# Optimization experiments

Measured on AMD Instinct MI355X. Metric: run time of the kernel, lower is better.

Reference implementation:

```python
import jax, jax.numpy as jnp
import numpy as np

B, L, DC, DQ, H = 32, 1024, 1024, 1024, 512
NEG_NUM = -10000.0


def setup_inputs() -> dict:
    key = jax.random.key(0)
    ks = jax.random.split(key, 7)
    s1 = 1.0 / np.sqrt(DC + DQ)
    s2 = 1.0 / np.sqrt(H)
    return {
        "ctx": jax.random.normal(ks[0], (B, L, DC), jnp.float32),
        "query": jax.random.normal(ks[1], (B, DQ), jnp.float32),
        "mask": jnp.ones((B, L), jnp.int32),
        "noise": jax.random.normal(ks[2], (B, L), jnp.float32),
        "W1": jax.random.uniform(ks[3], (DC + DQ, H), jnp.float32, -s1, s1),
        "b1": jax.random.uniform(ks[4], (H,), jnp.float32, -s1, s1),
        "w2": jax.random.uniform(ks[5], (H,), jnp.float32, -s2, s2),
        "b2": jnp.zeros((), jnp.float32),
    }


def reference(ctx, query, mask, noise, W1, b1, w2, b2):
    b, l, dc = ctx.shape
    # concat([ctx, query_expanded]) @ W1 == ctx @ W1[:DC] + query @ W1[DC:]
    hidden = jnp.tanh(
        jnp.einsum("blc,ch->blh", ctx, W1[:dc])
        + (query @ W1[dc:])[:, None, :]
        + b1
    )  # [B, L, H]
    score = hidden @ w2 + b2  # [B, L]
    score = jnp.where(mask == 0, NEG_NUM, score)
    score = score + noise  # sigmoid_noise=True -> coefficient 1
    p = jax.nn.sigmoid(score)  # p_choose_i [B, L]

    # initial prev_att: one-hot at position 0
    prev_att = jnp.zeros((b, l), score.dtype).at[:, 0].set(1.0)
    # shifted (1 - p): [1, 1-p_0, ..., 1-p_{L-2}]
    shifted = jnp.concatenate(
        [jnp.ones((b, 1), p.dtype), 1.0 - p[:, :-1]], axis=1
    )

    # linear recurrence a_t = shifted_t * a_{t-1} + prev_att_t  (a_{-1}=0)
    def step(carry, xs):
        s_t, pr_t = xs
        a = s_t * carry + pr_t
        return a, a

    _, att_t = jax.lax.scan(step, jnp.zeros((b,), p.dtype), (shifted.T, prev_att.T))
    att = att_t.T * p  # [B, L]

    expected_ctx = jnp.einsum("bl,blc->bc", att, ctx)  # bmm(p_ctx[:,None,:], ctx)
    return expected_ctx, att
```

## Files before the change

### kernel.cpp

```cpp
#include <hip/hip_runtime.h>
#include <hip/hip_bf16.h>
#include <math.h>

constexpr int Bb = 32;
constexpr int Ll = 1024;
constexpr int DC = 1024;
constexpr int DQ = 1024;
constexpr int Hh = 512;
#define NEG_NUM -10000.0f

typedef __attribute__((ext_vector_type(8))) short bf16x8;
typedef __attribute__((ext_vector_type(4))) float f32x4;

#define GLOAD_LDS16(g, l)                                                  \
    __builtin_amdgcn_global_load_lds(                                      \
        (const __attribute__((address_space(1))) void*)(g),                \
        (__attribute__((address_space(3))) void*)(l), 16, 0, 0)

__device__ inline unsigned short f2bf(float f) {
    unsigned int x = __float_as_uint(f);
    unsigned int r = (x + 0x7FFFu + ((x >> 16) & 1u)) >> 16;
    return (unsigned short)r;
}
__device__ inline float bfu(unsigned short u) {
    return __uint_as_float(((unsigned int)u) << 16);
}


__global__ __launch_bounds__(256) void prep_kernel(const float* __restrict__ W1,
                                                   const float* __restrict__ query,
                                                   const float* __restrict__ b1,
                                                   const float* __restrict__ ctx,
                                                   unsigned short* __restrict__ w1t,
                                                   float* __restrict__ qb,
                                                   float* __restrict__ score,
                                                   float* __restrict__ out_ctx,
                                                   unsigned short* __restrict__ ctxb) {
    __shared__ float red[4][64];
    const int bid = blockIdx.x;
    if (bid < 2048) {
        int idx = bid * 256 + threadIdx.x;
        int n = idx >> 10, k = idx & 1023;
        int ks = k ^ ((n & 7) << 3);
        w1t[(size_t)n * 1024 + ks] = f2bf(W1[(size_t)k * Hh + n]);
    } else if (bid < 2176) {
        int i = (bid - 2048) * 256 + threadIdx.x;
        out_ctx[i] = 0.f;
        score[i] = 0.f;
    } else if (bid < 2432) {
        const int qbid = bid - 2176;
        const int b  = qbid >> 3;
        const int hg = qbid & 7;
        const int hl = threadIdx.x & 63;
        const int j  = threadIdx.x >> 6;
        const int h  = hg * 64 + hl;
        const float* q = query + (size_t)b * DQ + j * 256;
        const float* w = W1 + (size_t)(DC + j * 256) * Hh + h;
        float a0 = 0.f, a1 = 0.f, a2 = 0.f, a3 = 0.f;
#pragma unroll 4
        for (int c = 0; c < 256; c += 4) {
            a0 += q[c + 0] * w[(size_t)(c + 0) * Hh];
            a1 += q[c + 1] * w[(size_t)(c + 1) * Hh];
            a2 += q[c + 2] * w[(size_t)(c + 2) * Hh];
            a3 += q[c + 3] * w[(size_t)(c + 3) * Hh];
        }
        red[j][hl] = (a0 + a1) + (a2 + a3);
        __syncthreads();
        if (j == 0)
            qb[(size_t)b * Hh + h] = red[0][hl] + red[1][hl] + red[2][hl] + red[3][hl] + b1[h];
    } else {
        size_t i = (size_t)((bid - 2432) * 256 + threadIdx.x) * 8;
        int row = (int)(i >> 10);
        int col = (int)(i & 1023);
        float4 v0 = *(const float4*)(ctx + i);
        float4 v1 = *(const float4*)(ctx + i + 4);
        union { unsigned short us[8]; uint4 v; } o;
        o.us[0] = f2bf(v0.x); o.us[1] = f2bf(v0.y); o.us[2] = f2bf(v0.z); o.us[3] = f2bf(v0.w);
        o.us[4] = f2bf(v1.x); o.us[5] = f2bf(v1.y); o.us[6] = f2bf(v1.z); o.us[7] = f2bf(v1.w);
        *(uint4*)(ctxb + ((size_t)row << 10) + (col ^ ((row & 7) << 3))) = o.v;
    }
}

__global__ __launch_bounds__(512, 1) void gemm_mfma(const unsigned short* __restrict__ ctxb,
                                                    const unsigned short* __restrict__ w1t,
                                                    const float* __restrict__ qb,
                                                    const float* __restrict__ w2,
                                                    float* __restrict__ score) {
    __shared__ unsigned short lds[2 * 32768];

    const int bid = blockIdx.x;
    const int n0 = ((bid >> 3) & 1) * 256;
    const int m0 = (((bid >> 4) << 3) | (bid & 7)) * 256;

    const int tid = threadIdx.x;
    const int wv = tid >> 6, lane = tid & 63;
    const int wr = wv >> 2, wc = wv & 3;
    const int lr = lane & 15, lk = lane >> 4;

    char* ldsB = (char*)lds;
    const char* ctxB = (const char*)ctxb;
    const char* w1tB = (const char*)w1t;

    const int srow = tid >> 3;
    const int scolb = (tid & 7) * 16;
    const int x = (lr & 7) << 4;

    f32x4 acc[8][4];
#pragma unroll
    for (int mf = 0; mf < 8; ++mf)
#pragma unroll
        for (int nf = 0; nf < 4; ++nf) acc[mf][nf] = (f32x4){0.f, 0.f, 0.f, 0.f};

#pragma unroll
    for (int i = 0; i < 4; ++i) {
        int row = i * 64 + srow;
        GLOAD_LDS16(ctxB + (size_t)(m0 + row) * 2048 + scolb,
                    ldsB + i * 8192 + tid * 16);
        GLOAD_LDS16(w1tB + (size_t)(n0 + row) * 2048 + scolb,
                    ldsB + 32768 + i * 8192 + tid * 16);
    }

    for (int ks = 0; ks < 16; ++ks) {
        const int cur = ks & 1;
        char* bufc = ldsB + cur * 65536;

        __builtin_amdgcn_s_barrier();
        if (ks < 15) {
            char* bufn = ldsB + (cur ^ 1) * 65536;
            const int kb = (ks + 1) * 128;
#pragma unroll
            for (int i = 0; i < 4; ++i) {
                int row = i * 64 + srow;
                GLOAD_LDS16(ctxB + (size_t)(m0 + row) * 2048 + kb + scolb,
                            bufn + i * 8192 + tid * 16);
                GLOAD_LDS16(w1tB + (size_t)(n0 + row) * 2048 + kb + scolb,
                            bufn + 32768 + i * 8192 + tid * 16);
            }
            asm volatile("s_waitcnt vmcnt(8)" ::: "memory");
        } else {
            asm volatile("s_waitcnt vmcnt(0)" ::: "memory");
        }
        __builtin_amdgcn_sched_barrier(0);
        __builtin_amdgcn_s_barrier();

#pragma unroll
        for (int kk = 0; kk < 2; ++kk) {
            const int colb = (kk * 64 + lk * 16) ^ x;
            bf16x8 a[8], bb[4];
#pragma unroll
            for (int nf = 0; nf < 4; ++nf)
                bb[nf] = *(const bf16x8*)(bufc + 32768 + (wc * 64 + nf * 16 + lr) * 128 + colb);
#pragma unroll
            for (int mf = 0; mf < 8; ++mf)
                a[mf] = *(const bf16x8*)(bufc + (wr * 128 + mf * 16 + lr) * 128 + colb);
#pragma unroll
            for (int mf = 0; mf < 8; ++mf)
#pragma unroll
                for (int nf = 0; nf < 4; ++nf)
                    acc[mf][nf] = __builtin_amdgcn_mfma_f32_16x16x32_bf16(a[mf], bb[nf], acc[mf][nf], 0, 0, 0);
        }
    }

    const int bq = m0 >> 10;
    const float* qbb = qb + (size_t)bq * Hh;
#pragma unroll
    for (int mf = 0; mf < 8; ++mf) {
        float s0 = 0.f, s1 = 0.f, s2 = 0.f, s3 = 0.f;
#pragma unroll
        for (int nf = 0; nf < 4; ++nf) {
            int col = n0 + wc * 64 + nf * 16 + lr;
            float wvw = w2[col];
            float qv = qbb[col];
            s0 += tanhf(acc[mf][nf][0] + qv) * wvw;
            s1 += tanhf(acc[mf][nf][1] + qv) * wvw;
            s2 += tanhf(acc[mf][nf][2] + qv) * wvw;
            s3 += tanhf(acc[mf][nf][3] + qv) * wvw;
        }
#pragma unroll
        for (int off = 8; off; off >>= 1) {
            s0 += __shfl_xor(s0, off, 16);
            s1 += __shfl_xor(s1, off, 16);
            s2 += __shfl_xor(s2, off, 16);
            s3 += __shfl_xor(s3, off, 16);
        }
        if (lr == 0) {
            int row = m0 + wr * 128 + mf * 16 + lk * 4;
            atomicAdd(&score[row + 0], s0);
            atomicAdd(&score[row + 1], s1);
            atomicAdd(&score[row + 2], s2);
            atomicAdd(&score[row + 3], s3);
        }
    }
}

__global__ __launch_bounds__(256) void ectx_fused(const unsigned short* __restrict__ ctxb,
                                                  const float* __restrict__ score,
                                                  const int* __restrict__ mask,
                                                  const float* __restrict__ noise,
                                                  const float* __restrict__ b2p,
                                                  float* __restrict__ att_out,
                                                  float* __restrict__ out) {
    __shared__ float att_s[1024];
    const int b = blockIdx.z;
    const int ly = blockIdx.y;
    const int tid = threadIdx.x;

    if (tid < 64) {
        const int lane = tid;
        const float b2 = b2p[0];
        const int base = b * Ll + lane * 16;
        float p[16], q[16];
        float run = 1.f;
#pragma unroll
        for (int j = 0; j < 16; ++j) {
            int l = base + j;
            float s = score[l] + b2;
            if (mask[l] == 0) s = NEG_NUM;
            s += noise[l];
            float pv = 1.f / (1.f + expf(-s));
            p[j] = pv;
            run *= (1.f - pv);
            q[j] = run;
        }
        float incl = run;
#pragma unroll
        for (int off = 1; off < 64; off <<= 1) {
            float v = __shfl_up(incl, off, 64);
            if (lane >= off) incl *= v;
        }
        float excl = __shfl_up(incl, 1, 64);
        if (lane == 0) excl = 1.f;
#pragma unroll
        for (int j = 0; j < 16; ++j) {
            float P = excl * (j == 0 ? 1.f : q[j - 1]);
            float av = p[j] * P;
            att_s[lane * 16 + j] = av;
            if (ly == 0) att_out[base + j] = av;
        }
    }
    __syncthreads();

    const int l0 = ly * 128;
    const unsigned short* cb = ctxb + ((size_t)b * Ll + l0) * DC;
    const int c = tid * 4;
    float a0 = 0.f, a1 = 0.f, a2 = 0.f, a3 = 0.f;
    for (int l = 0; l < 128; ++l) {
        float av = att_s[l0 + l];
        int cs = c ^ ((l & 7) << 3);
        ushort4 v = *(const ushort4*)(cb + (size_t)l * DC + cs);
        a0 += av * bfu(v.x); a1 += av * bfu(v.y);
        a2 += av * bfu(v.z); a3 += av * bfu(v.w);
    }
    float* o = out + (size_t)b * DC + c;
    atomicAdd(o + 0, a0); atomicAdd(o + 1, a1);
    atomicAdd(o + 2, a2); atomicAdd(o + 3, a3);
}

extern "C" void kernel_launch(void* const* d_in, const int* in_sizes, int n_in,
                              void* d_out, int out_size, void* d_ws, size_t ws_size,
                              hipStream_t stream) {
    const float* ctx   = (const float*)d_in[0];
    const float* query = (const float*)d_in[1];
    const int*   mask  = (const int*)d_in[2];
    const float* noise = (const float*)d_in[3];
    const float* W1    = (const float*)d_in[4];
    const float* b1    = (const float*)d_in[5];
    const float* w2    = (const float*)d_in[6];
    const float* b2    = (const float*)d_in[7];

    float* out_ctx = (float*)d_out;
    float* out_att = (float*)d_out + Bb * DC;

    char* ws = (char*)d_ws;
    float* score = (float*)ws;
    float* qb    = (float*)(ws + 131072);
    unsigned short* w1t  = (unsigned short*)(ws + 196608);
    unsigned short* ctxb = (unsigned short*)(ws + 1245184);

    prep_kernel<<<18816, 256, 0, stream>>>(W1, query, b1, ctx, w1t, qb, score, out_ctx, ctxb);

    gemm_mfma<<<256, 512, 0, stream>>>(ctxb, w1t, qb, w2, score);

    ectx_fused<<<dim3(1, Ll / 128, Bb), 256, 0, stream>>>(ctxb, score, mask, noise, b2,
                                                          out_att, out_ctx);
}
```

Baseline: 101.6 us.

## Use 4-stage K=64 LDS pipeline with row-paired swizzle and MFMA priority

Replaces the GEMM's double-buffered K=128 tiles with a four-buffer ring of K=64 tiles, keeping three stages of global-to-LDS loads in flight. The LDS layout packs two rows per 128-byte line with a new XOR swizzle, and the producer layouts of ctxb and w1t plus the consumer read in the final kernel are updated to match. It also raises wave priority around the MFMA block. The aim is to hide more memory latency and reduce LDS bank conflicts, at the cost of more barriers per K step and more complex addressing.

```diff
diff --git a/kernel.cpp b/kernel.cpp
--- a/kernel.cpp
+++ b/kernel.cpp
@@ -41,7 +41,7 @@
     if (bid < 2048) {
         int idx = bid * 256 + threadIdx.x;
         int n = idx >> 10, k = idx & 1023;
-        int ks = k ^ ((n & 7) << 3);
+        int ks = k ^ ((((n >> 1) & 3)) << 3);
         w1t[(size_t)n * 1024 + ks] = f2bf(W1[(size_t)k * Hh + n]);
     } else if (bid < 2176) {
         int i = (bid - 2048) * 256 + threadIdx.x;
@@ -77,7 +77,8 @@
         union { unsigned short us[8]; uint4 v; } o;
         o.us[0] = f2bf(v0.x); o.us[1] = f2bf(v0.y); o.us[2] = f2bf(v0.z); o.us[3] = f2bf(v0.w);
         o.us[4] = f2bf(v1.x); o.us[5] = f2bf(v1.y); o.us[6] = f2bf(v1.z); o.us[7] = f2bf(v1.w);
-        *(uint4*)(ctxb + ((size_t)row << 10) + (col ^ ((row & 7) << 3))) = o.v;
+        int cs = col ^ ((((row >> 1) & 3)) << 3);
+        *(uint4*)(ctxb + ((size_t)row << 10) + cs) = o.v;
     }
 }
 
@@ -86,7 +87,7 @@
                                                     const float* __restrict__ qb,
                                                     const float* __restrict__ w2,
                                                     float* __restrict__ score) {
-    __shared__ unsigned short lds[2 * 32768];
+    __shared__ unsigned short lds[4 * 16384];
 
     const int bid = blockIdx.x;
     const int n0 = ((bid >> 3) & 1) * 256;
@@ -101,9 +102,8 @@
     const char* ctxB = (const char*)ctxb;
     const char* w1tB = (const char*)w1t;
 
-    const int srow = tid >> 3;
-    const int scolb = (tid & 7) * 16;
-    const int x = (lr & 7) << 4;
+    const int sR = tid >> 3;
+    const int sp = tid & 7;
 
     f32x4 acc[8][4];
 #pragma unroll
@@ -111,54 +111,64 @@
 #pragma unroll
         for (int nf = 0; nf < 4; ++nf) acc[mf][nf] = (f32x4){0.f, 0.f, 0.f, 0.f};
 
-#pragma unroll
-    for (int i = 0; i < 4; ++i) {
-        int row = i * 64 + srow;
-        GLOAD_LDS16(ctxB + (size_t)(m0 + row) * 2048 + scolb,
-                    ldsB + i * 8192 + tid * 16);
-        GLOAD_LDS16(w1tB + (size_t)(n0 + row) * 2048 + scolb,
-                    ldsB + 32768 + i * 8192 + tid * 16);
-    }
-
-    for (int ks = 0; ks < 16; ++ks) {
-        const int cur = ks & 1;
-        char* bufc = ldsB + cur * 65536;
-
+#define STAGE_T(T)                                                             \
+    {                                                                          \
+        char* dst = ldsB + ((T) & 3) * 32768;                                  \
+        const int kb = ((T) >> 1) * 128 + ((T) & 1) * 64 + (sp & 3) * 16;      \
+        _Pragma("unroll")                                                      \
+        for (int i = 0; i < 2; ++i) {                                          \
+            int Rl = i * 64 + sR;                                              \
+            int mrow = m0 + 2 * Rl + (sp >> 2);                                \
+            int nrow = n0 + 2 * Rl + (sp >> 2);                                \
+            GLOAD_LDS16(ctxB + (size_t)mrow * 2048 + kb,                       \
+                        dst + i * 8192 + tid * 16);                            \
+            GLOAD_LDS16(w1tB + (size_t)nrow * 2048 + kb,                       \
+                        dst + 16384 + i * 8192 + tid * 16);                    \
+        }                                                                      \
+    }
+
+    STAGE_T(0); STAGE_T(1); STAGE_T(2);
+
+    for (int T = 0; T < 32; ++T) {
         __builtin_amdgcn_s_barrier();
-        if (ks < 15) {
-            char* bufn = ldsB + (cur ^ 1) * 65536;
-            const int kb = (ks + 1) * 128;
-#pragma unroll
-            for (int i = 0; i < 4; ++i) {
-                int row = i * 64 + srow;
-                GLOAD_LDS16(ctxB + (size_t)(m0 + row) * 2048 + kb + scolb,
-                            bufn + i * 8192 + tid * 16);
-                GLOAD_LDS16(w1tB + (size_t)(n0 + row) * 2048 + kb + scolb,
-                            bufn + 32768 + i * 8192 + tid * 16);
-            }
+        __builtin_amdgcn_sched_barrier(0);
+        if (T < 29) {
+            STAGE_T(T + 3);
+            asm volatile("s_waitcnt vmcnt(12)" ::: "memory");
+        } else if (T == 29) {
             asm volatile("s_waitcnt vmcnt(8)" ::: "memory");
+        } else if (T == 30) {
+            asm volatile("s_waitcnt vmcnt(4)" ::: "memory");
         } else {
             asm volatile("s_waitcnt vmcnt(0)" ::: "memory");
         }
         __builtin_amdgcn_sched_barrier(0);
         __builtin_amdgcn_s_barrier();
-
-#pragma unroll
-        for (int kk = 0; kk < 2; ++kk) {
-            const int colb = (kk * 64 + lk * 16) ^ x;
-            bf16x8 a[8], bb[4];
+        __builtin_amdgcn_sched_barrier(0);
+
+        const char* bufc = ldsB + (T & 3) * 32768;
+        bf16x8 a[8], bb[4];
+#pragma unroll
+        for (int nf = 0; nf < 4; ++nf) {
+            int nl = wc * 64 + nf * 16 + lr;
+            int R = nl >> 1;
+            bb[nf] = *(const bf16x8*)(bufc + 16384 + R * 128 +
+                                      ((nl & 1) * 4 + (lk ^ (R & 3))) * 16);
+        }
+#pragma unroll
+        for (int mf = 0; mf < 8; ++mf) {
+            int ml = wr * 128 + mf * 16 + lr;
+            int R = ml >> 1;
+            a[mf] = *(const bf16x8*)(bufc + R * 128 +
+                                     ((ml & 1) * 4 + (lk ^ (R & 3))) * 16);
+        }
+        __builtin_amdgcn_s_setprio(1);
+#pragma unroll
+        for (int mf = 0; mf < 8; ++mf)
 #pragma unroll
             for (int nf = 0; nf < 4; ++nf)
-                bb[nf] = *(const bf16x8*)(bufc + 32768 + (wc * 64 + nf * 16 + lr) * 128 + colb);
-#pragma unroll
-            for (int mf = 0; mf < 8; ++mf)
-                a[mf] = *(const bf16x8*)(bufc + (wr * 128 + mf * 16 + lr) * 128 + colb);
-#pragma unroll
-            for (int mf = 0; mf < 8; ++mf)
-#pragma unroll
-                for (int nf = 0; nf < 4; ++nf)
-                    acc[mf][nf] = __builtin_amdgcn_mfma_f32_16x16x32_bf16(a[mf], bb[nf], acc[mf][nf], 0, 0, 0);
-        }
+                acc[mf][nf] = __builtin_amdgcn_mfma_f32_16x16x32_bf16(a[mf], bb[nf], acc[mf][nf], 0, 0, 0);
+        __builtin_amdgcn_s_setprio(0);
     }
 
     const int bq = m0 >> 10;
@@ -246,7 +256,7 @@
     float a0 = 0.f, a1 = 0.f, a2 = 0.f, a3 = 0.f;
     for (int l = 0; l < 128; ++l) {
         float av = att_s[l0 + l];
-        int cs = c ^ ((l & 7) << 3);
+        int cs = c ^ (((((l0 + l) >> 1) & 3)) << 3);
         ushort4 v = *(const ushort4*)(cb + (size_t)l * DC + cs);
         a0 += av * bfu(v.x); a1 += av * bfu(v.y);
         a2 += av * bfu(v.z); a3 += av * bfu(v.w);
```

After: 104.6 us. +3.0%, slower.
